# Performance work log

Hardware: AMD Instinct MI355X
Metric: run time of the kernel (lower is better)

## Reference

```python
import jax, jax.numpy as jnp
import numpy as np

N = 50000
E = 800000
HID = 128
OUT = 64
HEADS = 4
NEG_SLOPE = 0.2


def gat_layer(x, edge_index, W, att_src, att_dst, bias):
    """PyG-style GATConv: shared linear for src/dst, additive attention,
    self-loops, segment softmax over incoming edges, concat heads + bias."""
    n = x.shape[0]
    H, C = att_src.shape
    # add self loops (PyG default add_self_loops=True)
    loops = jnp.arange(n, dtype=edge_index.dtype)
    src = jnp.concatenate([edge_index[0], loops])  # message sources j
    dst = jnp.concatenate([edge_index[1], loops])  # aggregation targets i
    xl = (x @ W).reshape(n, H, C)                  # [N,H,C]
    a_s = jnp.einsum('nhc,hc->nh', xl, att_src)    # [N,H]
    a_d = jnp.einsum('nhc,hc->nh', xl, att_dst)    # [N,H]
    e = jax.nn.leaky_relu(a_s[src] + a_d[dst], NEG_SLOPE)   # [E',H]
    m = jax.ops.segment_max(e, dst, num_segments=n)         # stable softmax
    e = jnp.exp(e - m[dst])
    denom = jax.ops.segment_sum(e, dst, num_segments=n)
    alpha = e / (denom[dst] + 1e-16)                        # [E',H]
    msg = xl[src] * alpha[:, :, None]                       # [E',H,C]
    out = jax.ops.segment_sum(msg, dst, num_segments=n)     # [N,H,C]
    return out.reshape(n, H * C) + bias


def setup_inputs() -> dict:
    key = jax.random.key(0)
    ks = jax.random.split(key, 16)
    C = HID // HEADS  # per-head channels = 32
    x = jax.random.normal(ks[0], (N, HID), dtype=jnp.float32)
    edge_indices = jax.random.randint(ks[1], (3, 2, E), 0, N, dtype=jnp.int32)
    s = 0.1
    inp = {
        'x': x,
        'edge_indices': edge_indices,
        'W1': jax.random.normal(ks[2], (HID, HEADS * C), dtype=jnp.float32) * s,
        'as1': jax.random.normal(ks[3], (HEADS, C), dtype=jnp.float32) * s,
        'ad1': jax.random.normal(ks[4], (HEADS, C), dtype=jnp.float32) * s,
        'b1': jnp.zeros((HEADS * C,), dtype=jnp.float32),
        'W2': jax.random.normal(ks[5], (HID, HEADS * C), dtype=jnp.float32) * s,
        'as2': jax.random.normal(ks[6], (HEADS, C), dtype=jnp.float32) * s,
        'ad2': jax.random.normal(ks[7], (HEADS, C), dtype=jnp.float32) * s,
        'b2': jnp.zeros((HEADS * C,), dtype=jnp.float32),
        'W3': jax.random.normal(ks[8], (HID, OUT), dtype=jnp.float32) * s,
        'as3': jax.random.normal(ks[9], (1, OUT), dtype=jnp.float32) * s,
        'ad3': jax.random.normal(ks[10], (1, OUT), dtype=jnp.float32) * s,
        'b3': jnp.zeros((OUT,), dtype=jnp.float32),
    }
    return inp


def reference(x, edge_indices, W1, as1, ad1, b1, W2, as2, ad2, b2, W3, as3, ad3, b3):
    h = jax.nn.relu(gat_layer(x, edge_indices[0], W1, as1, ad1, b1))
    h = jax.nn.relu(gat_layer(h, edge_indices[1], W2, as2, ad2, b2))
    out = gat_layer(h, edge_indices[2], W3, as3, ad3, b3)  # no ReLU on last layer
    return out
```

## Files before the change

### kernel.cpp

```cpp
#include <hip/hip_runtime.h>

typedef unsigned short u16;
typedef unsigned int u32;
typedef __attribute__((ext_vector_type(8))) short short8;
typedef __attribute__((ext_vector_type(4))) float f32x4;

#define HID 128

static inline int cdiv(long long a, int b) { return (int)((a + b - 1) / b); }

__device__ __forceinline__ float bfbits(u32 u) { union { u32 u; float f; } c; c.u = u; return c.f; }
__device__ __forceinline__ u16 f2bf(float f) {
  union { float f; u32 u; } c; c.f = f;
  u32 u = c.u;
  return (u16)((u + 0x7fffu + ((u >> 16) & 1u)) >> 16);
}
__device__ __forceinline__ u32 pack2bf(float a, float b) {
  return (u32)f2bf(a) | ((u32)f2bf(b) << 16);
}

template <int COUT, int HEADS, bool BF16IN>
__device__ __forceinline__ void gemm_body(
    int bx, int t, const void* __restrict__ HinV, const u16* __restrict__ WT,
    const float* __restrict__ attS, const float* __restrict__ attD,
    u16* __restrict__ XL, float* __restrict__ aS, float* __restrict__ aD, int n) {
  constexpr int NT = COUT / 16;
  constexpr int C = COUT / HEADS;
  constexpr int TPH = C / 16;

  int wv = t >> 6, ln = t & 63;
  int lrow = ln & 15;
  int lk = ln >> 4;
  int row = bx * 64 + wv * 16 + lrow;
  bool ok = (row < n);
  int rowc = ok ? row : (n - 1);

  short8 bb[4];
  if (BF16IN) {
    const u16* hp = (const u16*)HinV + (size_t)rowc * HID;
#pragma unroll
    for (int kb = 0; kb < 4; ++kb)
      bb[kb] = *(const short8*)(hp + kb * 32 + lk * 8);
  } else {
    const float* hp = (const float*)HinV + (size_t)rowc * HID;
    float4 hv[8];
#pragma unroll
    for (int kb = 0; kb < 4; ++kb) {
      hv[2 * kb] = *(const float4*)(hp + kb * 32 + lk * 8);
      hv[2 * kb + 1] = *(const float4*)(hp + kb * 32 + lk * 8 + 4);
    }
#pragma unroll
    for (int kb = 0; kb < 4; ++kb) {
      union { short8 s; u32 u[4]; } pk;
      float4 h0 = hv[2 * kb], h1 = hv[2 * kb + 1];
      pk.u[0] = pack2bf(h0.x, h0.y);
      pk.u[1] = pack2bf(h0.z, h0.w);
      pk.u[2] = pack2bf(h1.x, h1.y);
      pk.u[3] = pack2bf(h1.z, h1.w);
      bb[kb] = pk.s;
    }
  }

  f32x4 acc[NT];
#pragma unroll
  for (int ct = 0; ct < NT; ++ct) acc[ct] = {0.f, 0.f, 0.f, 0.f};

#pragma unroll
  for (int kb = 0; kb < 4; ++kb) {
    const u16* wp = WT + (size_t)lrow * HID + kb * 32 + lk * 8;
#pragma unroll
    for (int ct = 0; ct < NT; ++ct) {
      short8 aw = *(const short8*)(wp + (size_t)ct * 16 * HID);
      acc[ct] = __builtin_amdgcn_mfma_f32_16x16x32_bf16(aw, bb[kb], acc[ct], 0, 0, 0);
    }
  }

  float pS[HEADS], pD[HEADS];
#pragma unroll
  for (int h = 0; h < HEADS; ++h) { pS[h] = 0.f; pD[h] = 0.f; }
#pragma unroll
  for (int ct = 0; ct < NT; ++ct) {
    float4 sv = *(const float4*)(attS + ct * 16 + lk * 4);
    float4 dv = *(const float4*)(attD + ct * 16 + lk * 4);
    int h = ct / TPH;
    pS[h] += acc[ct][0] * sv.x + acc[ct][1] * sv.y + acc[ct][2] * sv.z + acc[ct][3] * sv.w;
    pD[h] += acc[ct][0] * dv.x + acc[ct][1] * dv.y + acc[ct][2] * dv.z + acc[ct][3] * dv.w;
  }
#pragma unroll
  for (int h = 0; h < HEADS; ++h) {
    pS[h] += __shfl_xor(pS[h], 16);
    pS[h] += __shfl_xor(pS[h], 32);
    pD[h] += __shfl_xor(pD[h], 16);
    pD[h] += __shfl_xor(pD[h], 32);
  }
  if (lk == 0 && ok) {
    if (HEADS == 4) {
      *(float4*)(aS + (size_t)row * 4) = make_float4(pS[0], pS[1], pS[2], pS[3]);
      *(float4*)(aD + (size_t)row * 4) = make_float4(pD[0], pD[1], pD[2], pD[3]);
    } else {
      aS[row] = pS[0];
      aD[row] = pD[0];
    }
  }

  if (ok) {
    u32* Xp = (u32*)XL + (size_t)row * (COUT / 2);
#pragma unroll
    for (int ct = 0; ct < NT; ++ct) {
      *(uint2*)(Xp + ct * 8 + lk * 2) =
          make_uint2(pack2bf(acc[ct][0], acc[ct][1]), pack2bf(acc[ct][2], acc[ct][3]));
    }
  }
}

template <int COUT, int HEADS, bool BF16IN>
__global__ __launch_bounds__(256) void gemm_attn_mfma(
    const void* __restrict__ HinV, const u16* __restrict__ WT,
    const float* __restrict__ attS, const float* __restrict__ attD,
    u16* __restrict__ XL, float* __restrict__ aS, float* __restrict__ aD, int n) {
  gemm_body<COUT, HEADS, BF16IN>(blockIdx.x, threadIdx.x, HinV, WT, attS, attD,
                                 XL, aS, aD, n);
}

#define PSTR 16

__global__ __launch_bounds__(256) void bucket_hist_prep(
    const int* __restrict__ ei, int* __restrict__ cntP, int e4, int rem, int E, int NB,
    const float* __restrict__ W1, const float* __restrict__ W2,
    const float* __restrict__ W3, u16* __restrict__ wt1, u16* __restrict__ wt2,
    u16* __restrict__ wt3) {
  if (blockIdx.y == 3) {
    int bx = blockIdx.x;
    if (bx >= 160) return;
    int y = (bx >= 128) ? 2 : (bx >= 64 ? 1 : 0);
    int b0 = (y == 0) ? 0 : ((y == 1) ? 64 : 128);
    const float* W = (y == 0) ? W1 : ((y == 1) ? W2 : W3);
    u16* WT = (y == 0) ? wt1 : ((y == 1) ? wt2 : wt3);
    int cout = (y == 2) ? 64 : 128;
    int idx = (bx - b0) * 256 + threadIdx.x;
    if (idx < 128 * cout) {
      int k = idx / cout, c = idx - k * cout;
      WT[c * 128 + k] = f2bf(W[idx]);
    }
    return;
  }
  int L = blockIdx.y;
  const int* dst = ei + (size_t)(2 * L + 1) * E;
  __shared__ int cnt[256];
  int t = threadIdx.x;
  cnt[t] = 0;
  __syncthreads();
  int gbase = blockIdx.x * 1024 + t;
#pragma unroll
  for (int u = 0; u < 4; ++u) {
    int g = gbase + u * 256;
    if (g < e4) {
      int4 d = *(const int4*)(dst + g * 4);
      atomicAdd(&cnt[d.x >> 8], 1);
      atomicAdd(&cnt[d.y >> 8], 1);
      atomicAdd(&cnt[d.z >> 8], 1);
      atomicAdd(&cnt[d.w >> 8], 1);
    }
  }
  if (blockIdx.x == 0 && t < rem) atomicAdd(&cnt[dst[e4 * 4 + t] >> 8], 1);
  __syncthreads();
  int c = cnt[t];
  if (t < NB && c > 0) atomicAdd(&cntP[(L * NB + t) * PSTR], c);
}

__global__ __launch_bounds__(256) void bucket_scan(const int* __restrict__ cntP,
                                                   int* __restrict__ bucketOff,
                                                   int* __restrict__ curP, int NB, int E) {
  int L = blockIdx.x;
  int t = threadIdx.x;
  int lane = t & 63, wid = t >> 6;
  __shared__ int wpart[4];
  int v = (t < NB) ? cntP[(L * NB + t) * PSTR] : 0;
  int inc = v;
#pragma unroll
  for (int off = 1; off < 64; off <<= 1) {
    int w = __shfl_up(inc, (unsigned)off, 64);
    if (lane >= off) inc += w;
  }
  if (lane == 63) wpart[wid] = inc;
  __syncthreads();
  if (t == 0) {
    int a = 0;
#pragma unroll
    for (int k = 0; k < 4; ++k) { int tmp = wpart[k]; wpart[k] = a; a += tmp; }
  }
  __syncthreads();
  int ex = wpart[wid] + inc - v;
  if (t < NB) {
    bucketOff[L * (NB + 1) + t] = ex;
    curP[(L * NB + t) * PSTR] = ex;
  }
  if (t == 0) bucketOff[L * (NB + 1) + NB] = E;
}

__global__ __launch_bounds__(256) void bucket_scatter_gemm(
    const int* __restrict__ ei, int* __restrict__ curP, u32* __restrict__ pairsAll,
    int e4, int rem, int E, int NB,
    const float* __restrict__ x, const u16* __restrict__ wt1,
    const float* __restrict__ as1, const float* __restrict__ ad1,
    u16* __restrict__ XL, float* __restrict__ aS, float* __restrict__ aD,
    int n, int ngb) {
  if (blockIdx.y == 3) {
    if ((int)blockIdx.x < ngb)
      gemm_body<128, 4, false>(blockIdx.x, threadIdx.x, x, wt1, as1, ad1, XL, aS, aD, n);
    return;
  }
  int L = blockIdx.y;
  const int* src = ei + (size_t)(2 * L) * E;
  const int* dst = src + E;
  u32* pairs = pairsAll + (size_t)L * E;
  __shared__ int cnt[256];
  __shared__ int baseS[256];
  int t = threadIdx.x;
  cnt[t] = 0;
  __syncthreads();

  int gbase = blockIdx.x * 1024 + t;
  int4 dv[4], sv[4];
  bool val[4];
#pragma unroll
  for (int u = 0; u < 4; ++u) {
    int g = gbase + u * 256;
    val[u] = (g < e4);
    if (val[u]) {
      dv[u] = *(const int4*)(dst + g * 4);
      sv[u] = *(const int4*)(src + g * 4);
      atomicAdd(&cnt[dv[u].x >> 8], 1);
      atomicAdd(&cnt[dv[u].y >> 8], 1);
      atomicAdd(&cnt[dv[u].z >> 8], 1);
      atomicAdd(&cnt[dv[u].w >> 8], 1);
    }
  }
  int tailS = 0, tailD = 0;
  bool hasTail = (blockIdx.x == 0 && t < rem);
  if (hasTail) {
    tailD = dst[e4 * 4 + t];
    tailS = src[e4 * 4 + t];
    atomicAdd(&cnt[tailD >> 8], 1);
  }
  __syncthreads();
  int c = cnt[t];
  if (t < NB && c > 0) baseS[t] = atomicAdd(&curP[(L * NB + t) * PSTR], c);
  __syncthreads();
  cnt[t] = 0;
  __syncthreads();
#pragma unroll
  for (int u = 0; u < 4; ++u) {
    if (val[u]) {
      int b, p;
      b = dv[u].x >> 8; p = atomicAdd(&cnt[b], 1);
      pairs[baseS[b] + p] = ((u32)(dv[u].x & 0xff) << 24) | (u32)sv[u].x;
      b = dv[u].y >> 8; p = atomicAdd(&cnt[b], 1);
      pairs[baseS[b] + p] = ((u32)(dv[u].y & 0xff) << 24) | (u32)sv[u].y;
      b = dv[u].z >> 8; p = atomicAdd(&cnt[b], 1);
      pairs[baseS[b] + p] = ((u32)(dv[u].z & 0xff) << 24) | (u32)sv[u].z;
      b = dv[u].w >> 8; p = atomicAdd(&cnt[b], 1);
      pairs[baseS[b] + p] = ((u32)(dv[u].w & 0xff) << 24) | (u32)sv[u].w;
    }
  }
  if (hasTail) {
    int b = tailD >> 8;
    int p = atomicAdd(&cnt[b], 1);
    pairs[baseS[b] + p] = ((u32)(tailD & 0xff) << 24) | (u32)tailS;
  }
}

__global__ __launch_bounds__(256) void csr_finalize(const u32* __restrict__ pairsAll,
                                                    const int* __restrict__ bucketOff,
                                                    int* __restrict__ indptrAll,
                                                    int* __restrict__ srcIdxAll,
                                                    int N, int E, int NB) {
  int L = blockIdx.y, b = blockIdx.x;
  const u32* pairs = pairsAll + (size_t)L * E;
  int* indptr = indptrAll + (size_t)L * (N + 1);
  int* srcL = srcIdxAll + (size_t)L * (E + N);
  int base = b << 8;
  int nodes = min(256, N - base);
  int p0 = bucketOff[L * (NB + 1) + b];
  int p1 = bucketOff[L * (NB + 1) + b + 1];

  __shared__ int cnt[256];
  __shared__ int wpart[4];
  int t = threadIdx.x;
  int lane = t & 63, wid = t >> 6;
  cnt[t] = 0;
  __syncthreads();

  for (int i = p0 + t; i < p1; i += 256) atomicAdd(&cnt[pairs[i] >> 24], 1);
  __syncthreads();

  int v = (t < nodes) ? cnt[t] + 1 : 0;
  int inc = v;
#pragma unroll
  for (int off = 1; off < 64; off <<= 1) {
    int w = __shfl_up(inc, (unsigned)off, 64);
    if (lane >= off) inc += w;
  }
  if (lane == 63) wpart[wid] = inc;
  __syncthreads();
  if (t == 0) {
    int a = 0;
#pragma unroll
    for (int k = 0; k < 4; ++k) { int tmp = wpart[k]; wpart[k] = a; a += tmp; }
  }
  __syncthreads();
  int ex = wpart[wid] + inc - v;
  __syncthreads();
  if (t < nodes) {
    int segStart = p0 + base + ex;
    indptr[base + t] = segStart;
    srcL[segStart] = base + t;
    cnt[t] = segStart + 1;
  }
  if (b == NB - 1 && t == 0) indptr[N] = E + N;
  __syncthreads();

  for (int i = p0 + t; i < p1; i += 256) {
    u32 pk = pairs[i];
    int p = atomicAdd(&cnt[pk >> 24], 1);
    srcL[p] = (int)(pk & 0xffffffu);
  }
}

template <int COUT, int HEADS, bool RELU, bool OUTBF>
__global__ __launch_bounds__(256, 8) void aggregate(
    const u16* __restrict__ XL, const float* __restrict__ aS, const float* __restrict__ aD,
    const int* __restrict__ indptr, const int* __restrict__ srcIdx,
    const float* __restrict__ bias, void* __restrict__ outV, int n) {
  constexpr int LPN = COUT / 8;
  constexpr int NPW = 64 / LPN;
  constexpr int C = COUT / HEADS;
  constexpr int D = 4;

  int wid = (blockIdx.x * blockDim.x + threadIdx.x) >> 6;
  int lane = threadIdx.x & 63;
  int sub = lane / LPN;
  int cl = lane % LPN;
  int i = wid * NPW + sub;
  bool ok = (i < n);
  int ic = ok ? i : (n - 1);

  int col0 = cl * 8;
  int h = col0 / C;
  float ad = aD[(size_t)ic * HEADS + h];
  int e0 = indptr[ic];
  int deg = indptr[ic + 1] - e0;

  const u32* XL32 = (const u32*)XL;
  float s = 0.f;
  float acc[8];
#pragma unroll
  for (int v = 0; v < 8; ++v) acc[v] = 0.f;

  auto fetch = [&](int k, float& av, uint4& q) {
    int kk = (k < deg) ? k : 0;
    int j = srcIdx[e0 + kk];
    av = aS[(size_t)j * HEADS + h];
    q = *(const uint4*)(XL32 + (size_t)j * (COUT / 2) + cl * 4);
  };
  auto consume = [&](int k, float av, const uint4& q) {
    if (k >= deg) return;
    float l = av + ad;
    l = (l >= 0.f) ? l : 0.2f * l;
    float el = __expf(fminf(l, 60.f));
    s += el;
    acc[0] += el * bfbits(q.x << 16);
    acc[1] += el * bfbits(q.x & 0xffff0000u);
    acc[2] += el * bfbits(q.y << 16);
    acc[3] += el * bfbits(q.y & 0xffff0000u);
    acc[4] += el * bfbits(q.z << 16);
    acc[5] += el * bfbits(q.z & 0xffff0000u);
    acc[6] += el * bfbits(q.w << 16);
    acc[7] += el * bfbits(q.w & 0xffff0000u);
  };

  float aP[D];
  uint4 qP[D];
#pragma unroll
  for (int j = 0; j < D; ++j) fetch(j, aP[j], qP[j]);

  for (int k0 = 0; k0 < deg; k0 += D) {
    bool more = (k0 + D < deg);
#pragma unroll
    for (int j = 0; j < D; ++j) {
      float av = aP[j];
      uint4 q = qP[j];
      if (more) fetch(k0 + D + j, aP[j], qP[j]);
      consume(k0 + j, av, q);
    }
  }

  if (!ok) return;
  float inv = 1.f / (s + 1e-16f);
  float o[8];
#pragma unroll
  for (int v = 0; v < 8; ++v) {
    o[v] = acc[v] * inv + bias[col0 + v];
    if (RELU) o[v] = fmaxf(o[v], 0.f);
  }
  if (OUTBF) {
    u32* op = (u32*)outV + (size_t)i * (COUT / 2) + cl * 4;
    *(uint4*)op = make_uint4(pack2bf(o[0], o[1]), pack2bf(o[2], o[3]),
                             pack2bf(o[4], o[5]), pack2bf(o[6], o[7]));
  } else {
    float* op = (float*)outV + (size_t)i * COUT + col0;
    *(float4*)op = make_float4(o[0], o[1], o[2], o[3]);
    *(float4*)(op + 4) = make_float4(o[4], o[5], o[6], o[7]);
  }
}

extern "C" void kernel_launch(void* const* d_in, const int* in_sizes, int n_in,
                              void* d_out, int out_size, void* d_ws, size_t ws_size,
                              hipStream_t stream) {
  const float* x = (const float*)d_in[0];
  const int* ei = (const int*)d_in[1];
  const float* W1 = (const float*)d_in[2];
  const float* as1 = (const float*)d_in[3];
  const float* ad1 = (const float*)d_in[4];
  const float* b1 = (const float*)d_in[5];
  const float* W2 = (const float*)d_in[6];
  const float* as2 = (const float*)d_in[7];
  const float* ad2 = (const float*)d_in[8];
  const float* b2 = (const float*)d_in[9];
  const float* W3 = (const float*)d_in[10];
  const float* as3 = (const float*)d_in[11];
  const float* ad3 = (const float*)d_in[12];
  const float* b3 = (const float*)d_in[13];

  int N = in_sizes[0] / HID;
  int E = in_sizes[1] / 6;
  int NB = cdiv(N, 256);

  char* w = (char*)d_ws;
  auto alloc = [&](size_t bytes) {
    void* q = (void*)w;
    w += (bytes + 255) & ~(size_t)255;
    return q;
  };
  u16* bufH = (u16*)alloc((size_t)N * HID * 2);
  u16* bufXL = (u16*)alloc((size_t)N * HID * 2);
  float* aS = (float*)alloc((size_t)N * 4 * 4);
  float* aD = (float*)alloc((size_t)N * 4 * 4);
  u16* wt1 = (u16*)alloc((size_t)128 * 128 * 2);
  u16* wt2 = (u16*)alloc((size_t)128 * 128 * 2);
  u16* wt3 = (u16*)alloc((size_t)64 * 128 * 2);
  int* cntP = (int*)alloc((size_t)3 * NB * PSTR * 4);
  int* curP = (int*)alloc((size_t)3 * NB * PSTR * 4);
  int* bucketOff = (int*)alloc((size_t)3 * (NB + 1) * 4);
  u32* pairsAll = (u32*)alloc((size_t)3 * E * 4);
  int* indptrAll = (int*)alloc((size_t)3 * (N + 1) * 4);
  int* srcIdxAll = (int*)alloc((size_t)3 * (E + N) * 4);

  int e4 = E >> 2, rem = E & 3;
  int gx = cdiv(e4, 1024);
  int ngb = cdiv(N, 64);
  int gxh = (gx > 160) ? gx : 160;
  int gxs = (gx > ngb) ? gx : ngb;

  hipMemsetAsync(cntP, 0, (size_t)3 * NB * PSTR * 4, stream);
  {
    dim3 g(gxh, 4);
    bucket_hist_prep<<<g, 256, 0, stream>>>(ei, cntP, e4, rem, E, NB,
                                            W1, W2, W3, wt1, wt2, wt3);
  }
  bucket_scan<<<3, 256, 0, stream>>>(cntP, bucketOff, curP, NB, E);
  {
    dim3 g(gxs, 4);
    bucket_scatter_gemm<<<g, 256, 0, stream>>>(ei, curP, pairsAll, e4, rem, E, NB,
                                               x, wt1, as1, ad1, bufXL, aS, aD, N, ngb);
  }
  {
    dim3 g(NB, 3);
    csr_finalize<<<g, 256, 0, stream>>>(pairsAll, bucketOff, indptrAll, srcIdxAll, N, E, NB);
  }

  aggregate<128, 4, true, true><<<cdiv(N, 16), 256, 0, stream>>>(
      bufXL, aS, aD, indptrAll, srcIdxAll, b1, bufH, N);
  gemm_attn_mfma<128, 4, true><<<cdiv(N, 64), 256, 0, stream>>>(
      bufH, wt2, as2, ad2, bufXL, aS, aD, N);
  aggregate<128, 4, true, true><<<cdiv(N, 16), 256, 0, stream>>>(
      bufXL, aS, aD, indptrAll + (N + 1), srcIdxAll + (size_t)(E + N), b2, bufH, N);
  gemm_attn_mfma<64, 1, true><<<cdiv(N, 64), 256, 0, stream>>>(
      bufH, wt3, as3, ad3, bufXL, aS, aD, N);
  aggregate<64, 1, false, false><<<cdiv(N, 32), 256, 0, stream>>>(
      bufXL, aS, aD, indptrAll + 2 * (N + 1), srcIdxAll + (size_t)2 * (E + N), b3,
      d_out, N);
}
```

Measured before the change: 323.5 us.

## Store projected features in column-sliced layout and aggregate per slice

The GEMM now writes XL transposed into 16-column slices ([slice][node][16] bf16), and aggregation launches one block per (slice, 128-node group), with two threads per node each covering 8 columns. The aim is that each slice's gather working set (N*32 bytes) fits in L2, which should cut the cost of random gathers. In exchange, the edge index list and attention logits are re-read once per slice and exp is recomputed per slice. The prefetch depth also drops from 4 to 1, which exposes more latency per thread.

```diff
diff --git a/kernel.cpp b/kernel.cpp
--- a/kernel.cpp
+++ b/kernel.cpp
@@ -23,7 +23,7 @@
 __device__ __forceinline__ void gemm_body(
     int bx, int t, const void* __restrict__ HinV, const u16* __restrict__ WT,
     const float* __restrict__ attS, const float* __restrict__ attD,
-    u16* __restrict__ XL, float* __restrict__ aS, float* __restrict__ aD, int n) {
+    u16* __restrict__ XLt, float* __restrict__ aS, float* __restrict__ aD, int n) {
   constexpr int NT = COUT / 16;
   constexpr int C = COUT / HEADS;
   constexpr int TPH = C / 16;
@@ -104,10 +104,10 @@
   }
 
   if (ok) {
-    u32* Xp = (u32*)XL + (size_t)row * (COUT / 2);
 #pragma unroll
     for (int ct = 0; ct < NT; ++ct) {
-      *(uint2*)(Xp + ct * 8 + lk * 2) =
+      u32* p = (u32*)(XLt + ((size_t)ct * n + row) * 16);
+      *(uint2*)(p + lk * 2) =
           make_uint2(pack2bf(acc[ct][0], acc[ct][1]), pack2bf(acc[ct][2], acc[ct][3]));
     }
   }
@@ -117,9 +117,9 @@
 __global__ __launch_bounds__(256) void gemm_attn_mfma(
     const void* __restrict__ HinV, const u16* __restrict__ WT,
     const float* __restrict__ attS, const float* __restrict__ attD,
-    u16* __restrict__ XL, float* __restrict__ aS, float* __restrict__ aD, int n) {
+    u16* __restrict__ XLt, float* __restrict__ aS, float* __restrict__ aD, int n) {
   gemm_body<COUT, HEADS, BF16IN>(blockIdx.x, threadIdx.x, HinV, WT, attS, attD,
-                                 XL, aS, aD, n);
+                                 XLt, aS, aD, n);
 }
 
 #define PSTR 16
@@ -203,11 +203,11 @@
     int e4, int rem, int E, int NB,
     const float* __restrict__ x, const u16* __restrict__ wt1,
     const float* __restrict__ as1, const float* __restrict__ ad1,
-    u16* __restrict__ XL, float* __restrict__ aS, float* __restrict__ aD,
+    u16* __restrict__ XLt, float* __restrict__ aS, float* __restrict__ aD,
     int n, int ngb) {
   if (blockIdx.y == 3) {
     if ((int)blockIdx.x < ngb)
-      gemm_body<128, 4, false>(blockIdx.x, threadIdx.x, x, wt1, as1, ad1, XL, aS, aD, n);
+      gemm_body<128, 4, false>(blockIdx.x, threadIdx.x, x, wt1, as1, ad1, XLt, aS, aD, n);
     return;
   }
   int L = blockIdx.y;
@@ -328,75 +328,63 @@
 }
 
 template <int COUT, int HEADS, bool RELU, bool OUTBF>
-__global__ __launch_bounds__(256, 8) void aggregate(
-    const u16* __restrict__ XL, const float* __restrict__ aS, const float* __restrict__ aD,
+__global__ __launch_bounds__(256, 8) void aggregate_sliced(
+    const u16* __restrict__ XLt, const float* __restrict__ aS, const float* __restrict__ aD,
     const int* __restrict__ indptr, const int* __restrict__ srcIdx,
     const float* __restrict__ bias, void* __restrict__ outV, int n) {
-  constexpr int LPN = COUT / 8;
-  constexpr int NPW = 64 / LPN;
+  constexpr int SLICES = COUT / 16;
   constexpr int C = COUT / HEADS;
-  constexpr int D = 4;
-
-  int wid = (blockIdx.x * blockDim.x + threadIdx.x) >> 6;
-  int lane = threadIdx.x & 63;
-  int sub = lane / LPN;
-  int cl = lane % LPN;
-  int i = wid * NPW + sub;
-  bool ok = (i < n);
-  int ic = ok ? i : (n - 1);
-
-  int col0 = cl * 8;
-  int h = col0 / C;
+  constexpr int NPB = 128;
+
+  int slice = blockIdx.x % SLICES;
+  int nb = blockIdx.x / SLICES;
+  int t = threadIdx.x;
+  int pairId = t >> 1;
+  int half = t & 1;
+  int node = nb * NPB + pairId;
+  bool ok = (node < n);
+  int ic = ok ? node : (n - 1);
+
+  int h = (slice * 16) / C;
   float ad = aD[(size_t)ic * HEADS + h];
   int e0 = indptr[ic];
   int deg = indptr[ic + 1] - e0;
 
-  const u32* XL32 = (const u32*)XL;
+  const u16* xbase = XLt + (size_t)slice * n * 16;
   float s = 0.f;
   float acc[8];
 #pragma unroll
   for (int v = 0; v < 8; ++v) acc[v] = 0.f;
 
-  auto fetch = [&](int k, float& av, uint4& q) {
-    int kk = (k < deg) ? k : 0;
-    int j = srcIdx[e0 + kk];
-    av = aS[(size_t)j * HEADS + h];
-    q = *(const uint4*)(XL32 + (size_t)j * (COUT / 2) + cl * 4);
-  };
-  auto consume = [&](int k, float av, const uint4& q) {
-    if (k >= deg) return;
-    float l = av + ad;
+  int j = srcIdx[e0];
+  float an = aS[(size_t)j * HEADS + h];
+  uint4 qn = *(const uint4*)(xbase + (size_t)j * 16 + half * 8);
+
+  for (int k = 0; k < deg; ++k) {
+    float ac = an;
+    uint4 qc = qn;
+    if (k + 1 < deg) {
+      int j2 = srcIdx[e0 + k + 1];
+      an = aS[(size_t)j2 * HEADS + h];
+      qn = *(const uint4*)(xbase + (size_t)j2 * 16 + half * 8);
+    }
+    float l = ac + ad;
     l = (l >= 0.f) ? l : 0.2f * l;
     float el = __expf(fminf(l, 60.f));
     s += el;
-    acc[0] += el * bfbits(q.x << 16);
-    acc[1] += el * bfbits(q.x & 0xffff0000u);
-    acc[2] += el * bfbits(q.y << 16);
-    acc[3] += el * bfbits(q.y & 0xffff0000u);
-    acc[4] += el * bfbits(q.z << 16);
-    acc[5] += el * bfbits(q.z & 0xffff0000u);
-    acc[6] += el * bfbits(q.w << 16);
-    acc[7] += el * bfbits(q.w & 0xffff0000u);
-  };
-
-  float aP[D];
-  uint4 qP[D];
-#pragma unroll
-  for (int j = 0; j < D; ++j) fetch(j, aP[j], qP[j]);
-
-  for (int k0 = 0; k0 < deg; k0 += D) {
-    bool more = (k0 + D < deg);
-#pragma unroll
-    for (int j = 0; j < D; ++j) {
-      float av = aP[j];
-      uint4 q = qP[j];
-      if (more) fetch(k0 + D + j, aP[j], qP[j]);
-      consume(k0 + j, av, q);
-    }
+    acc[0] += el * bfbits(qc.x << 16);
+    acc[1] += el * bfbits(qc.x & 0xffff0000u);
+    acc[2] += el * bfbits(qc.y << 16);
+    acc[3] += el * bfbits(qc.y & 0xffff0000u);
+    acc[4] += el * bfbits(qc.z << 16);
+    acc[5] += el * bfbits(qc.z & 0xffff0000u);
+    acc[6] += el * bfbits(qc.w << 16);
+    acc[7] += el * bfbits(qc.w & 0xffff0000u);
   }
 
   if (!ok) return;
   float inv = 1.f / (s + 1e-16f);
+  int col0 = slice * 16 + half * 8;
   float o[8];
 #pragma unroll
   for (int v = 0; v < 8; ++v) {
@@ -404,11 +392,11 @@
     if (RELU) o[v] = fmaxf(o[v], 0.f);
   }
   if (OUTBF) {
-    u32* op = (u32*)outV + (size_t)i * (COUT / 2) + cl * 4;
+    u32* op = (u32*)outV + (size_t)node * (COUT / 2) + (col0 >> 1);
     *(uint4*)op = make_uint4(pack2bf(o[0], o[1]), pack2bf(o[2], o[3]),
                              pack2bf(o[4], o[5]), pack2bf(o[6], o[7]));
   } else {
-    float* op = (float*)outV + (size_t)i * COUT + col0;
+    float* op = (float*)outV + (size_t)node * COUT + col0;
     *(float4*)op = make_float4(o[0], o[1], o[2], o[3]);
     *(float4*)(op + 4) = make_float4(o[4], o[5], o[6], o[7]);
   }
@@ -479,15 +467,15 @@
     csr_finalize<<<g, 256, 0, stream>>>(pairsAll, bucketOff, indptrAll, srcIdxAll, N, E, NB);
   }
 
-  aggregate<128, 4, true, true><<<cdiv(N, 16), 256, 0, stream>>>(
+  aggregate_sliced<128, 4, true, true><<<8 * cdiv(N, 128), 256, 0, stream>>>(
       bufXL, aS, aD, indptrAll, srcIdxAll, b1, bufH, N);
   gemm_attn_mfma<128, 4, true><<<cdiv(N, 64), 256, 0, stream>>>(
       bufH, wt2, as2, ad2, bufXL, aS, aD, N);
-  aggregate<128, 4, true, true><<<cdiv(N, 16), 256, 0, stream>>>(
+  aggregate_sliced<128, 4, true, true><<<8 * cdiv(N, 128), 256, 0, stream>>>(
       bufXL, aS, aD, indptrAll + (N + 1), srcIdxAll + (size_t)(E + N), b2, bufH, N);
   gemm_attn_mfma<64, 1, true><<<cdiv(N, 64), 256, 0, stream>>>(
       bufH, wt3, as3, ad3, bufXL, aS, aD, N);
-  aggregate<64, 1, false, false><<<cdiv(N, 32), 256, 0, stream>>>(
+  aggregate_sliced<64, 1, false, false><<<4 * cdiv(N, 128), 256, 0, stream>>>(
       bufXL, aS, aD, indptrAll + 2 * (N + 1), srcIdxAll + (size_t)2 * (E + N), b3,
       d_out, N);
 }
```

Result: slower. 435.3 us (+34.6%).

## Precompute per-edge attention weights in separate kernel and unfuse prep kernels

Applied to the files above, without the earlier changes.

Adds an edge_w kernel that computes the exponentiated leaky-ReLU attention logit for every CSR edge and head, and stores it in a head-major buffer. The aggregate kernels then read those weights with vectorized int4/float4 loads instead of gathering aS and evaluating exp inline. The weight-transpose and layer-1 GEMM work that was folded into the histogram and scatter kernels is split back into standalone launches. The aim is to simplify the gather loop, but it adds a per-layer write and read of an (E+N)×heads weight buffer. edge_w also walks each node's edges serially with uncoalesced stores, and there are more kernel launches with less overlap.

```diff
diff --git a/kernel.cpp b/kernel.cpp
--- a/kernel.cpp
+++ b/kernel.cpp
@@ -19,19 +19,35 @@
   return (u32)f2bf(a) | ((u32)f2bf(b) << 16);
 }
 
+__global__ __launch_bounds__(256) void prep_wt3(
+    const float* __restrict__ W1, const float* __restrict__ W2,
+    const float* __restrict__ W3, u16* __restrict__ wt1, u16* __restrict__ wt2,
+    u16* __restrict__ wt3) {
+  int y = blockIdx.y;
+  const float* W = (y == 0) ? W1 : ((y == 1) ? W2 : W3);
+  u16* WT = (y == 0) ? wt1 : ((y == 1) ? wt2 : wt3);
+  int cout = (y == 2) ? 64 : 128;
+  int idx = blockIdx.x * 256 + threadIdx.x;
+  if (idx < 128 * cout) {
+    int k = idx / cout, c = idx - k * cout;
+    WT[c * 128 + k] = f2bf(W[idx]);
+  }
+}
+
 template <int COUT, int HEADS, bool BF16IN>
-__device__ __forceinline__ void gemm_body(
-    int bx, int t, const void* __restrict__ HinV, const u16* __restrict__ WT,
+__global__ __launch_bounds__(256) void gemm_attn_mfma(
+    const void* __restrict__ HinV, const u16* __restrict__ WT,
     const float* __restrict__ attS, const float* __restrict__ attD,
     u16* __restrict__ XL, float* __restrict__ aS, float* __restrict__ aD, int n) {
   constexpr int NT = COUT / 16;
   constexpr int C = COUT / HEADS;
   constexpr int TPH = C / 16;
 
+  int t = threadIdx.x;
   int wv = t >> 6, ln = t & 63;
   int lrow = ln & 15;
   int lk = ln >> 4;
-  int row = bx * 64 + wv * 16 + lrow;
+  int row = blockIdx.x * 64 + wv * 16 + lrow;
   bool ok = (row < n);
   int rowc = ok ? row : (n - 1);
 
@@ -113,37 +129,11 @@
   }
 }
 
-template <int COUT, int HEADS, bool BF16IN>
-__global__ __launch_bounds__(256) void gemm_attn_mfma(
-    const void* __restrict__ HinV, const u16* __restrict__ WT,
-    const float* __restrict__ attS, const float* __restrict__ attD,
-    u16* __restrict__ XL, float* __restrict__ aS, float* __restrict__ aD, int n) {
-  gemm_body<COUT, HEADS, BF16IN>(blockIdx.x, threadIdx.x, HinV, WT, attS, attD,
-                                 XL, aS, aD, n);
-}
-
 #define PSTR 16
 
-__global__ __launch_bounds__(256) void bucket_hist_prep(
-    const int* __restrict__ ei, int* __restrict__ cntP, int e4, int rem, int E, int NB,
-    const float* __restrict__ W1, const float* __restrict__ W2,
-    const float* __restrict__ W3, u16* __restrict__ wt1, u16* __restrict__ wt2,
-    u16* __restrict__ wt3) {
-  if (blockIdx.y == 3) {
-    int bx = blockIdx.x;
-    if (bx >= 160) return;
-    int y = (bx >= 128) ? 2 : (bx >= 64 ? 1 : 0);
-    int b0 = (y == 0) ? 0 : ((y == 1) ? 64 : 128);
-    const float* W = (y == 0) ? W1 : ((y == 1) ? W2 : W3);
-    u16* WT = (y == 0) ? wt1 : ((y == 1) ? wt2 : wt3);
-    int cout = (y == 2) ? 64 : 128;
-    int idx = (bx - b0) * 256 + threadIdx.x;
-    if (idx < 128 * cout) {
-      int k = idx / cout, c = idx - k * cout;
-      WT[c * 128 + k] = f2bf(W[idx]);
-    }
-    return;
-  }
+__global__ __launch_bounds__(256) void bucket_hist(const int* __restrict__ ei,
+                                                   int* __restrict__ cntP,
+                                                   int e4, int rem, int E, int NB) {
   int L = blockIdx.y;
   const int* dst = ei + (size_t)(2 * L + 1) * E;
   __shared__ int cnt[256];
@@ -198,18 +188,10 @@
   if (t == 0) bucketOff[L * (NB + 1) + NB] = E;
 }
 
-__global__ __launch_bounds__(256) void bucket_scatter_gemm(
-    const int* __restrict__ ei, int* __restrict__ curP, u32* __restrict__ pairsAll,
-    int e4, int rem, int E, int NB,
-    const float* __restrict__ x, const u16* __restrict__ wt1,
-    const float* __restrict__ as1, const float* __restrict__ ad1,
-    u16* __restrict__ XL, float* __restrict__ aS, float* __restrict__ aD,
-    int n, int ngb) {
-  if (blockIdx.y == 3) {
-    if ((int)blockIdx.x < ngb)
-      gemm_body<128, 4, false>(blockIdx.x, threadIdx.x, x, wt1, as1, ad1, XL, aS, aD, n);
-    return;
-  }
+__global__ __launch_bounds__(256) void bucket_scatter(const int* __restrict__ ei,
+                                                      int* __restrict__ curP,
+                                                      u32* __restrict__ pairsAll,
+                                                      int e4, int rem, int E, int NB) {
   int L = blockIdx.y;
   const int* src = ei + (size_t)(2 * L) * E;
   const int* dst = src + E;
@@ -327,15 +309,36 @@
   }
 }
 
+template <int HEADS>
+__global__ __launch_bounds__(256) void edge_w(
+    const float* __restrict__ aS, const float* __restrict__ aD,
+    const int* __restrict__ indptr, const int* __restrict__ srcIdx,
+    float* __restrict__ wOut, int n, int wstride) {
+  int i = blockIdx.x * 256 + threadIdx.x;
+  if (i >= n) return;
+  float ad[HEADS];
+#pragma unroll
+  for (int h = 0; h < HEADS; ++h) ad[h] = aD[(size_t)i * HEADS + h];
+  int e0 = indptr[i], e1 = indptr[i + 1];
+  for (int e = e0; e < e1; ++e) {
+    int j = srcIdx[e];
+#pragma unroll
+    for (int h = 0; h < HEADS; ++h) {
+      float l = aS[(size_t)j * HEADS + h] + ad[h];
+      l = (l >= 0.f) ? l : 0.2f * l;
+      wOut[(size_t)h * wstride + e] = __expf(fminf(l, 60.f));
+    }
+  }
+}
+
 template <int COUT, int HEADS, bool RELU, bool OUTBF>
 __global__ __launch_bounds__(256, 8) void aggregate(
-    const u16* __restrict__ XL, const float* __restrict__ aS, const float* __restrict__ aD,
+    const u16* __restrict__ XL, const float* __restrict__ wAll,
     const int* __restrict__ indptr, const int* __restrict__ srcIdx,
-    const float* __restrict__ bias, void* __restrict__ outV, int n) {
+    const float* __restrict__ bias, void* __restrict__ outV, int n, int wstride) {
   constexpr int LPN = COUT / 8;
   constexpr int NPW = 64 / LPN;
   constexpr int C = COUT / HEADS;
-  constexpr int D = 4;
 
   int wid = (blockIdx.x * blockDim.x + threadIdx.x) >> 6;
   int lane = threadIdx.x & 63;
@@ -347,27 +350,17 @@
 
   int col0 = cl * 8;
   int h = col0 / C;
-  float ad = aD[(size_t)ic * HEADS + h];
   int e0 = indptr[ic];
   int deg = indptr[ic + 1] - e0;
-
+  const float* wh = wAll + (size_t)h * wstride;
   const u32* XL32 = (const u32*)XL;
+
   float s = 0.f;
   float acc[8];
 #pragma unroll
   for (int v = 0; v < 8; ++v) acc[v] = 0.f;
 
-  auto fetch = [&](int k, float& av, uint4& q) {
-    int kk = (k < deg) ? k : 0;
-    int j = srcIdx[e0 + kk];
-    av = aS[(size_t)j * HEADS + h];
-    q = *(const uint4*)(XL32 + (size_t)j * (COUT / 2) + cl * 4);
-  };
-  auto consume = [&](int k, float av, const uint4& q) {
-    if (k >= deg) return;
-    float l = av + ad;
-    l = (l >= 0.f) ? l : 0.2f * l;
-    float el = __expf(fminf(l, 60.f));
+  auto cons = [&](float el, const uint4& q) {
     s += el;
     acc[0] += el * bfbits(q.x << 16);
     acc[1] += el * bfbits(q.x & 0xffff0000u);
@@ -378,21 +371,49 @@
     acc[6] += el * bfbits(q.w << 16);
     acc[7] += el * bfbits(q.w & 0xffff0000u);
   };
-
-  float aP[D];
-  uint4 qP[D];
-#pragma unroll
-  for (int j = 0; j < D; ++j) fetch(j, aP[j], qP[j]);
-
-  for (int k0 = 0; k0 < deg; k0 += D) {
-    bool more = (k0 + D < deg);
-#pragma unroll
-    for (int j = 0; j < D; ++j) {
-      float av = aP[j];
-      uint4 q = qP[j];
-      if (more) fetch(k0 + D + j, aP[j], qP[j]);
-      consume(k0 + j, av, q);
-    }
+  auto xlrow = [&](int j) {
+    return *(const uint4*)(XL32 + (size_t)j * (COUT / 2) + cl * 4);
+  };
+
+  int nbF = deg >> 2;
+  int r = deg & 3;
+
+  int4 jA;
+  float4 wA;
+  if (nbF > 0) {
+    jA = *(const int4*)(srcIdx + e0);
+    wA = *(const float4*)(wh + e0);
+  }
+  for (int b = 0; b < nbF; ++b) {
+    int4 jC = jA;
+    float4 wC = wA;
+    if (b + 1 < nbF) {
+      jA = *(const int4*)(srcIdx + e0 + (b + 1) * 4);
+      wA = *(const float4*)(wh + e0 + (b + 1) * 4);
+    }
+    uint4 q0 = xlrow(jC.x);
+    uint4 q1 = xlrow(jC.y);
+    uint4 q2 = xlrow(jC.z);
+    uint4 q3 = xlrow(jC.w);
+    cons(wC.x, q0);
+    cons(wC.y, q1);
+    cons(wC.z, q2);
+    cons(wC.w, q3);
+  }
+  if (r) {
+    int e = e0 + nbF * 4;
+    int j0 = srcIdx[e];
+    int j1 = (r > 1) ? srcIdx[e + 1] : 0;
+    int j2 = (r > 2) ? srcIdx[e + 2] : 0;
+    float w0 = wh[e];
+    float w1 = (r > 1) ? wh[e + 1] : 0.f;
+    float w2 = (r > 2) ? wh[e + 2] : 0.f;
+    uint4 q0 = xlrow(j0);
+    uint4 q1 = xlrow(j1);
+    uint4 q2 = xlrow(j2);
+    cons(w0, q0);
+    if (r > 1) cons(w1, q1);
+    if (r > 2) cons(w2, q2);
   }
 
   if (!ok) return;
@@ -435,6 +456,7 @@
   int N = in_sizes[0] / HID;
   int E = in_sizes[1] / 6;
   int NB = cdiv(N, 256);
+  int EN = E + N;
 
   char* w = (char*)d_ws;
   auto alloc = [&](size_t bytes) {
@@ -446,6 +468,7 @@
   u16* bufXL = (u16*)alloc((size_t)N * HID * 2);
   float* aS = (float*)alloc((size_t)N * 4 * 4);
   float* aD = (float*)alloc((size_t)N * 4 * 4);
+  float* wEdge = (float*)alloc((size_t)4 * EN * 4);
   u16* wt1 = (u16*)alloc((size_t)128 * 128 * 2);
   u16* wt2 = (u16*)alloc((size_t)128 * 128 * 2);
   u16* wt3 = (u16*)alloc((size_t)64 * 128 * 2);
@@ -454,40 +477,47 @@
   int* bucketOff = (int*)alloc((size_t)3 * (NB + 1) * 4);
   u32* pairsAll = (u32*)alloc((size_t)3 * E * 4);
   int* indptrAll = (int*)alloc((size_t)3 * (N + 1) * 4);
-  int* srcIdxAll = (int*)alloc((size_t)3 * (E + N) * 4);
+  int* srcIdxAll = (int*)alloc((size_t)3 * EN * 4);
 
   int e4 = E >> 2, rem = E & 3;
   int gx = cdiv(e4, 1024);
-  int ngb = cdiv(N, 64);
-  int gxh = (gx > 160) ? gx : 160;
-  int gxs = (gx > ngb) ? gx : ngb;
-
+  int ngn = cdiv(N, 256);
+
+  {
+    dim3 g(64, 3);
+    prep_wt3<<<g, 256, 0, stream>>>(W1, W2, W3, wt1, wt2, wt3);
+  }
   hipMemsetAsync(cntP, 0, (size_t)3 * NB * PSTR * 4, stream);
   {
-    dim3 g(gxh, 4);
-    bucket_hist_prep<<<g, 256, 0, stream>>>(ei, cntP, e4, rem, E, NB,
-                                            W1, W2, W3, wt1, wt2, wt3);
+    dim3 g(gx, 3);
+    bucket_hist<<<g, 256, 0, stream>>>(ei, cntP, e4, rem, E, NB);
   }
   bucket_scan<<<3, 256, 0, stream>>>(cntP, bucketOff, curP, NB, E);
   {
-    dim3 g(gxs, 4);
-    bucket_scatter_gemm<<<g, 256, 0, stream>>>(ei, curP, pairsAll, e4, rem, E, NB,
-                                               x, wt1, as1, ad1, bufXL, aS, aD, N, ngb);
+    dim3 g(gx, 3);
+    bucket_scatter<<<g, 256, 0, stream>>>(ei, curP, pairsAll, e4, rem, E, NB);
   }
   {
     dim3 g(NB, 3);
     csr_finalize<<<g, 256, 0, stream>>>(pairsAll, bucketOff, indptrAll, srcIdxAll, N, E, NB);
   }
 
+  gemm_attn_mfma<128, 4, false><<<cdiv(N, 64), 256, 0, stream>>>(
+      x, wt1, as1, ad1, bufXL, aS, aD, N);
+  edge_w<4><<<ngn, 256, 0, stream>>>(aS, aD, indptrAll, srcIdxAll, wEdge, N, EN);
   aggregate<128, 4, true, true><<<cdiv(N, 16), 256, 0, stream>>>(
-      bufXL, aS, aD, indptrAll, srcIdxAll, b1, bufH, N);
+      bufXL, wEdge, indptrAll, srcIdxAll, b1, bufH, N, EN);
   gemm_attn_mfma<128, 4, true><<<cdiv(N, 64), 256, 0, stream>>>(
       bufH, wt2, as2, ad2, bufXL, aS, aD, N);
+  edge_w<4><<<ngn, 256, 0, stream>>>(aS, aD, indptrAll + (N + 1),
+                                     srcIdxAll + (size_t)EN, wEdge, N, EN);
   aggregate<128, 4, true, true><<<cdiv(N, 16), 256, 0, stream>>>(
-      bufXL, aS, aD, indptrAll + (N + 1), srcIdxAll + (size_t)(E + N), b2, bufH, N);
+      bufXL, wEdge, indptrAll + (N + 1), srcIdxAll + (size_t)EN, b2, bufH, N, EN);
   gemm_attn_mfma<64, 1, true><<<cdiv(N, 64), 256, 0, stream>>>(
       bufH, wt3, as3, ad3, bufXL, aS, aD, N);
+  edge_w<1><<<ngn, 256, 0, stream>>>(aS, aD, indptrAll + 2 * (N + 1),
+                                     srcIdxAll + (size_t)2 * EN, wEdge, N, EN);
   aggregate<64, 1, false, false><<<cdiv(N, 32), 256, 0, stream>>>(
-      bufXL, aS, aD, indptrAll + 2 * (N + 1), srcIdxAll + (size_t)2 * (E + N), b3,
-      d_out, N);
-}
+      bufXL, wEdge, indptrAll + 2 * (N + 1), srcIdxAll + (size_t)2 * EN, b3,
+      d_out, N, EN);
+}
```

New measurement: 408.1 us. 1.26x slower.
